# Optimization experiments

Measured on AMD Instinct MI355X. Metric: run time of the kernel, lower is better.

## Reference

```python
import jax, jax.numpy as jnp
import numpy as np

# ---- Cl(4,1) Cayley table (conformal GA: metric +,+,+,+,-) ----
_METRIC = (1.0, 1.0, 1.0, 1.0, -1.0)

def _reorder_sign(a, b):
    # sign from counting swaps to bring blade product to canonical order
    a >>= 1
    s = 0
    while a:
        s += bin(a & b).count("1")
        a >>= 1
    return -1.0 if (s & 1) else 1.0

def _build_cayley():
    C = np.zeros((32, 32, 32), dtype=np.float32)
    for a in range(32):
        for b in range(32):
            s = _reorder_sign(a, b)
            common = a & b
            for i in range(5):
                if (common >> i) & 1:
                    s *= _METRIC[i]
            C[a, b, a ^ b] += s
    return C

CAYLEY = _build_cayley()  # [32,32,32]; out_k = sum_ij C[i,j,k] x_i y_j

EPS = 1e-8

def normalize_cl41(x):
    n = jnp.sqrt(jnp.sum(x * x, axis=-1, keepdims=True))
    return x / (n + EPS)


def setup_inputs() -> dict:
    key = jax.random.key(0)
    k_x, k_wi, k_bi, k_wo, k_bo = jax.random.split(key, 5)
    B, S, D, H = 64, 2048, 6, 8
    x = jax.random.normal(k_x, (B, S, D), dtype=jnp.float32)
    W_in = jax.random.normal(k_wi, (D, H * 32), dtype=jnp.float32) * (1.0 / np.sqrt(D))
    b_in = jax.random.normal(k_bi, (H * 32,), dtype=jnp.float32) * 0.01
    W_out = jax.random.normal(k_wo, (H * 32, 32), dtype=jnp.float32) * (1.0 / np.sqrt(H * 32))
    b_out = jax.random.normal(k_bo, (32,), dtype=jnp.float32) * 0.01
    return {"x": x, "W_in": W_in, "b_in": b_in, "W_out": W_out, "b_out": b_out}


def reference(x, W_in, b_in, W_out, b_out):
    B, S, D = x.shape
    H = W_in.shape[1] // 32
    C = jnp.asarray(CAYLEY)
    # project inputs to per-channel multivectors: (B,S,H,32)
    u = (x @ W_in + b_in).reshape(B, S, H, 32)
    # initial rotor state: identity (scalar blade = 1)
    psi0 = jnp.zeros((B, H, 32), dtype=x.dtype).at[..., 0].set(1.0)

    def step(psi, u_t):  # u_t: (B,H,32)
        delta = normalize_cl41(u_t.at[..., 0].add(1.0))
        psi = normalize_cl41(jnp.einsum("bhi,bhj,ijk->bhk", delta, psi, C))
        return psi, psi

    _, psi_seq = jax.lax.scan(step, psi0, jnp.swapaxes(u, 0, 1))  # (S,B,H,32)
    out = normalize_cl41(psi_seq.reshape(S, B, H * 32) @ W_out + b_out)  # (S,B,32)
    return jnp.swapaxes(out, 0, 1)  # (B,S,32)
```

## Files before the change

### kernel.cpp

```cpp
#include <hip/hip_runtime.h>
#include <hip/hip_bf16.h>
#include <stdint.h>

#define BB 64
#define SS 2048
#define DD 6
#define HH 8
#define NCH 512
#define CHUNKS 256
#define LCH 8

typedef unsigned short ushort_t;
typedef __attribute__((ext_vector_type(8))) __bf16 bf16x8;
typedef __attribute__((ext_vector_type(4))) float f32x4;

struct SignTab { float s[32][32]; };

constexpr int popc5_c(unsigned v) {
    int c = 0;
    for (int i = 0; i < 5; ++i) c += (v >> i) & 1u;
    return c;
}

constexpr SignTab make_signs() {
    SignTab t{};
    for (int a = 0; a < 32; ++a) {
        for (int b = 0; b < 32; ++b) {
            int cnt = 0;
            unsigned aa = ((unsigned)a) >> 1;
            while (aa) { cnt += popc5_c(aa & (unsigned)b); aa >>= 1; }
            if ((a & b) & 16) cnt += 1;
            t.s[a][b] = (cnt & 1) ? -1.0f : 1.0f;
        }
    }
    return t;
}

constexpr SignTab SGN = make_signs();

__device__ __forceinline__ void gp_cl41(const float* __restrict__ a,
                                        const float* __restrict__ b,
                                        float* __restrict__ o) {
#pragma unroll
    for (int k = 0; k < 32; ++k) o[k] = 0.0f;
#pragma unroll
    for (int i = 0; i < 32; ++i) {
#pragma unroll
        for (int k = 0; k < 32; ++k) {
            o[k] = fmaf(SGN.s[i][i ^ k] * a[i], b[i ^ k], o[k]);
        }
    }
}

__device__ __forceinline__ float sumsq32(const float* v) {
    float n0 = 0.f, n1 = 0.f, n2 = 0.f, n3 = 0.f;
#pragma unroll
    for (int k = 0; k < 32; k += 4) {
        n0 = fmaf(v[k+0], v[k+0], n0);
        n1 = fmaf(v[k+1], v[k+1], n1);
        n2 = fmaf(v[k+2], v[k+2], n2);
        n3 = fmaf(v[k+3], v[k+3], n3);
    }
    return (n0 + n1) + (n2 + n3);
}

__device__ __forceinline__ float rsq(float n) {
    return __builtin_amdgcn_rsqf(n);
}

__device__ __forceinline__ uint32_t f2bf_rne(float f) {
    uint32_t u = __float_as_uint(f);
    return (u + 0x7FFFu + ((u >> 16) & 1u)) >> 16;
}

__device__ __forceinline__ uint32_t packh2(float a, float b) {
    union { _Float16 h[2]; uint32_t u; } t;
    t.h[0] = (_Float16)a; t.h[1] = (_Float16)b;
    return t.u;
}
__device__ __forceinline__ float h2lo(uint32_t u) {
    union { uint32_t u32; _Float16 h[2]; } t; t.u32 = u; return (float)t.h[0];
}
__device__ __forceinline__ float h2hi(uint32_t u) {
    union { uint32_t u32; _Float16 h[2]; } t; t.u32 = u; return (float)t.h[1];
}

__global__ __launch_bounds__(256) void k_local(
        const float* __restrict__ x, const float* __restrict__ W_in,
        const float* __restrict__ b_in, ushort_t* __restrict__ psi_loc,
        float* __restrict__ Tbuf) {
    __shared__ float4 sW4[8][57];
    for (int idx = threadIdx.x; idx < 8 * 56; idx += 256) {
        int h = idx / 56, r = idx % 56;
        float4 v;
        if (r < 48) {
            int d = r / 8, j4 = r % 8;
            const float* p = W_in + d * 256 + h * 32 + 4 * j4;
            v = make_float4(p[0], p[1], p[2], p[3]);
        } else {
            const float* p = b_in + h * 32 + 4 * (r - 48);
            v = make_float4(p[0], p[1], p[2], p[3]);
        }
        sW4[h][r] = v;
    }
    __syncthreads();

    int tid = blockIdx.x * 256 + threadIdx.x;
    int c  = tid >> 9;
    int bh = tid & 511;
    int b = bh >> 3, h = bh & 7;

    float4 bias4[8];
#pragma unroll
    for (int j4 = 0; j4 < 8; ++j4) bias4[j4] = sW4[h][48 + j4];

    float p[32];
#pragma unroll
    for (int k = 0; k < 32; ++k) p[k] = 0.f;
    p[0] = 1.f;

    const float* xrow = x + ((size_t)b * SS + (size_t)c * LCH) * DD;
    ushort_t* psi_base = psi_loc + (((size_t)b * SS + (size_t)c * LCH) * HH + h) * 32;

#pragma unroll 1
    for (int pr = 0; pr < LCH / 2; ++pr) {
        float xv[12];
#pragma unroll
        for (int d = 0; d < 6; ++d) {
            float2 t2 = *(const float2*)(xrow + 2 * d);
            xv[2 * d] = t2.x; xv[2 * d + 1] = t2.y;
        }
        xrow += 12;
        float x0[6], x1[6];
#pragma unroll
        for (int d = 0; d < 6; ++d) { x0[d] = xv[d]; x1[d] = xv[6 + d]; }

        float dl0[32], dl1[32];
#pragma unroll
        for (int j4 = 0; j4 < 8; ++j4) {
            float4 bv = bias4[j4];
            dl0[4*j4+0] = bv.x; dl0[4*j4+1] = bv.y; dl0[4*j4+2] = bv.z; dl0[4*j4+3] = bv.w;
            dl1[4*j4+0] = bv.x; dl1[4*j4+1] = bv.y; dl1[4*j4+2] = bv.z; dl1[4*j4+3] = bv.w;
        }
#pragma unroll
        for (int d = 0; d < 6; ++d) {
            float a0 = x0[d], a1 = x1[d];
#pragma unroll
            for (int j4 = 0; j4 < 8; ++j4) {
                float4 w = sW4[h][d * 8 + j4];
                dl0[4*j4+0] = fmaf(a0, w.x, dl0[4*j4+0]);
                dl0[4*j4+1] = fmaf(a0, w.y, dl0[4*j4+1]);
                dl0[4*j4+2] = fmaf(a0, w.z, dl0[4*j4+2]);
                dl0[4*j4+3] = fmaf(a0, w.w, dl0[4*j4+3]);
                dl1[4*j4+0] = fmaf(a1, w.x, dl1[4*j4+0]);
                dl1[4*j4+1] = fmaf(a1, w.y, dl1[4*j4+1]);
                dl1[4*j4+2] = fmaf(a1, w.z, dl1[4*j4+2]);
                dl1[4*j4+3] = fmaf(a1, w.w, dl1[4*j4+3]);
            }
        }
        dl0[0] += 1.0f;
        dl1[0] += 1.0f;

        float o[32];
        gp_cl41(dl0, p, o);
        {
            float inv = rsq(sumsq32(o));
            ushort_t* dst = psi_base + (size_t)(2 * pr) * HH * 32;
            uint32_t pk[16];
#pragma unroll
            for (int m = 0; m < 16; ++m)
                pk[m] = packh2(o[2*m] * inv, o[2*m+1] * inv);
            uint4* d4 = (uint4*)dst;
#pragma unroll
            for (int m = 0; m < 4; ++m)
                d4[m] = make_uint4(pk[4*m], pk[4*m+1], pk[4*m+2], pk[4*m+3]);
        }
        gp_cl41(dl1, o, p);
        {
            float inv = rsq(sumsq32(p));
            ushort_t* dst = psi_base + (size_t)(2 * pr + 1) * HH * 32;
            uint32_t pk[16];
#pragma unroll
            for (int m = 0; m < 16; ++m)
                pk[m] = packh2(p[2*m] * inv, p[2*m+1] * inv);
            uint4* d4 = (uint4*)dst;
#pragma unroll
            for (int m = 0; m < 4; ++m)
                d4[m] = make_uint4(pk[4*m], pk[4*m+1], pk[4*m+2], pk[4*m+3]);
        }
    }

    float inv = rsq(sumsq32(p));
    float* dst = Tbuf + ((size_t)bh * CHUNKS + c) * 32;
#pragma unroll
    for (int k = 0; k < 32; ++k) dst[k] = p[k] * inv;
}

__global__ __launch_bounds__(256) void k_scan_totals(
        const float* __restrict__ Tbuf, float* __restrict__ Ebuf) {
    __shared__ float sT[CHUNKS][33];
    int chain = blockIdx.x;
    int c = threadIdx.x;

    float v[32];
    const float* src = Tbuf + ((size_t)chain * CHUNKS + c) * 32;
#pragma unroll
    for (int k = 0; k < 32; ++k) { v[k] = src[k]; sT[c][k] = v[k]; }
    __syncthreads();

#pragma unroll 1
    for (int off = 1; off < CHUNKS; off <<= 1) {
        float w[32];
        bool act = (c >= off);
        if (act) {
#pragma unroll
            for (int k = 0; k < 32; ++k) w[k] = sT[c - off][k];
        }
        __syncthreads();
        if (act) {
            float o[32];
            gp_cl41(v, w, o);
            float inv = rsq(sumsq32(o));
#pragma unroll
            for (int k = 0; k < 32; ++k) { v[k] = o[k] * inv; sT[c][k] = v[k]; }
        }
        __syncthreads();
    }

    float* dst = Ebuf + (size_t)chain * CHUNKS * 32;
    if (c == 0) {
#pragma unroll
        for (int k = 0; k < 32; ++k) dst[k] = (k == 0) ? 1.f : 0.f;
    }
    if (c < CHUNKS - 1) {
        float* d2 = dst + (size_t)(c + 1) * 32;
#pragma unroll
        for (int k = 0; k < 32; ++k) d2[k] = v[k];
    }
}

__global__ __launch_bounds__(256) void k_fixup_proj(
        const ushort_t* __restrict__ psi_loc, const float* __restrict__ Ebuf,
        const float* __restrict__ W_out, const float* __restrict__ b_out,
        float* __restrict__ out) {
    int lane = threadIdx.x & 63;
    int wv = threadIdx.x >> 6;
    int q = lane >> 4;
    int n0 = lane & 15;

    bf16x8 Bf[2][8];
#pragma unroll
    for (int nt = 0; nt < 2; ++nt)
#pragma unroll
        for (int kk = 0; kk < 8; ++kk) {
            union { ushort_t u[8]; bf16x8 v; } tmp;
#pragma unroll
            for (int j = 0; j < 8; ++j)
                tmp.u[j] = (ushort_t)f2bf_rne(W_out[(kk * 32 + q * 8 + j) * 32 + nt * 16 + n0]);
            Bf[nt][kk] = tmp.v;
        }
    float bn0 = b_out[n0], bn1 = b_out[16 + n0];

    __shared__ ushort_t psiT[4][16][264];

#pragma unroll 1
    for (int tile = blockIdx.x * 4 + wv; tile < 8192; tile += 2048) {
        int rr0 = tile * 16;
        int b = rr0 >> 11;
        int s0 = rr0 & 2047;

        __syncthreads();

#pragma unroll
        for (int pp = 0; pp < 2; ++pp) {
            int row_local = pp * 8 + (lane >> 3);
            int h = lane & 7;
            int s = s0 + row_local;
            int c = s >> 3;
            int bh = b * 8 + h;

            float a[32], w[32], o[32];
            const uint4* pl = (const uint4*)(psi_loc +
                    (((size_t)b * SS + s) * HH + h) * 32);
#pragma unroll
            for (int m = 0; m < 4; ++m) {
                uint4 t4 = pl[m];
                uint32_t uu[4] = { t4.x, t4.y, t4.z, t4.w };
#pragma unroll
                for (int z = 0; z < 4; ++z) {
                    a[8*m + 2*z]     = h2lo(uu[z]);
                    a[8*m + 2*z + 1] = h2hi(uu[z]);
                }
            }
            const float* e = Ebuf + ((size_t)bh * CHUNKS + c) * 32;
#pragma unroll
            for (int k = 0; k < 32; ++k) w[k] = e[k];

            gp_cl41(a, w, o);
            float inv = rsq(sumsq32(o));

            uint32_t pk[16];
#pragma unroll
            for (int m = 0; m < 16; ++m)
                pk[m] = f2bf_rne(o[2*m] * inv) | (f2bf_rne(o[2*m+1] * inv) << 16);
            uint4* dst = (uint4*)&psiT[wv][row_local][h * 32];
#pragma unroll
            for (int m = 0; m < 4; ++m)
                dst[m] = make_uint4(pk[4*m], pk[4*m+1], pk[4*m+2], pk[4*m+3]);
        }

        __syncthreads();

        f32x4 acc0 = {0.f, 0.f, 0.f, 0.f};
        f32x4 acc1 = {0.f, 0.f, 0.f, 0.f};
#pragma unroll
        for (int kk = 0; kk < 8; ++kk) {
            bf16x8 af = *(const bf16x8*)&psiT[wv][n0][kk * 32 + q * 8];
            acc0 = __builtin_amdgcn_mfma_f32_16x16x32_bf16(af, Bf[0][kk], acc0, 0, 0, 0);
            acc1 = __builtin_amdgcn_mfma_f32_16x16x32_bf16(af, Bf[1][kk], acc1, 0, 0, 0);
        }

        float c0[4], c1[4], ss[4];
#pragma unroll
        for (int i = 0; i < 4; ++i) {
            c0[i] = acc0[i] + bn0;
            c1[i] = acc1[i] + bn1;
            ss[i] = c0[i] * c0[i] + c1[i] * c1[i];
        }
#pragma unroll
        for (int m = 1; m < 16; m <<= 1) {
#pragma unroll
            for (int i = 0; i < 4; ++i) ss[i] += __shfl_xor(ss[i], m);
        }
#pragma unroll
        for (int i = 0; i < 4; ++i) {
            float inv = rsq(ss[i]);
            int row = rr0 + q * 4 + i;
            out[(size_t)row * 32 + n0]      = c0[i] * inv;
            out[(size_t)row * 32 + 16 + n0] = c1[i] * inv;
        }
    }
}

extern "C" void kernel_launch(void* const* d_in, const int* in_sizes, int n_in,
                              void* d_out, int out_size, void* d_ws, size_t ws_size,
                              hipStream_t stream) {
    const float* x     = (const float*)d_in[0];
    const float* W_in  = (const float*)d_in[1];
    const float* b_in  = (const float*)d_in[2];
    const float* W_out = (const float*)d_in[3];
    const float* b_out = (const float*)d_in[4];
    float* out = (float*)d_out;

    char* ws = (char*)d_ws;
    float* Tbuf = (float*)ws;
    float* Ebuf = Tbuf;
    ushort_t* psi = (ushort_t*)(ws + (size_t)16 * 1024 * 1024);

    k_local      <<<512, 256, 0, stream>>>(x, W_in, b_in, psi, Tbuf);
    k_scan_totals<<<512, 256, 0, stream>>>(Tbuf, Ebuf);
    k_fixup_proj <<<512, 256, 0, stream>>>(psi, Ebuf, W_out, b_out, out);
}
```

Baseline: 204.0 us.

## Fuse local chunk scan into totals scan and recompute chains in projection kernel

The three-kernel pipeline becomes two. The first kernel computes each chunk's local product and the block-level prefix scan in one launch, so the Tbuf round trip is gone. The second kernel starts from the chunk prefix and recomputes the within-chunk chain, then feeds the results straight into the MFMA output projection. This removes the fp16 psi_loc intermediate, avoiding its global write and read and its precision loss, at the cost of running the geometric-product chain twice and adding more __syncthreads in small 64-thread blocks.

```diff
diff --git a/kernel.cpp b/kernel.cpp
--- a/kernel.cpp
+++ b/kernel.cpp
@@ -73,180 +73,179 @@
     return (u + 0x7FFFu + ((u >> 16) & 1u)) >> 16;
 }
 
-__device__ __forceinline__ uint32_t packh2(float a, float b) {
-    union { _Float16 h[2]; uint32_t u; } t;
-    t.h[0] = (_Float16)a; t.h[1] = (_Float16)b;
-    return t.u;
-}
-__device__ __forceinline__ float h2lo(uint32_t u) {
-    union { uint32_t u32; _Float16 h[2]; } t; t.u32 = u; return (float)t.h[0];
-}
-__device__ __forceinline__ float h2hi(uint32_t u) {
-    union { uint32_t u32; _Float16 h[2]; } t; t.u32 = u; return (float)t.h[1];
-}
-
-__global__ __launch_bounds__(256) void k_local(
+__device__ __forceinline__ void make_delta(const float4* __restrict__ sW,
+                                           const float* __restrict__ x6,
+                                           float* __restrict__ dl) {
+#pragma unroll
+    for (int j4 = 0; j4 < 8; ++j4) {
+        float4 bv = sW[48 + j4];
+        dl[4*j4+0] = bv.x; dl[4*j4+1] = bv.y; dl[4*j4+2] = bv.z; dl[4*j4+3] = bv.w;
+    }
+#pragma unroll
+    for (int d = 0; d < 6; ++d) {
+        float a = x6[d];
+#pragma unroll
+        for (int j4 = 0; j4 < 8; ++j4) {
+            float4 w = sW[d * 8 + j4];
+            dl[4*j4+0] = fmaf(a, w.x, dl[4*j4+0]);
+            dl[4*j4+1] = fmaf(a, w.y, dl[4*j4+1]);
+            dl[4*j4+2] = fmaf(a, w.z, dl[4*j4+2]);
+            dl[4*j4+3] = fmaf(a, w.w, dl[4*j4+3]);
+        }
+    }
+    dl[0] += 1.0f;
+}
+
+__global__ __launch_bounds__(256, 2) void k_scan(
         const float* __restrict__ x, const float* __restrict__ W_in,
-        const float* __restrict__ b_in, ushort_t* __restrict__ psi_loc,
-        float* __restrict__ Tbuf) {
+        const float* __restrict__ b_in, float* __restrict__ Ebuf) {
+    __shared__ float4 sW4[57];
+    __shared__ float sT[CHUNKS][36];
+
+    int chain = blockIdx.x;
+    int b = chain >> 3, h = chain & 7;
+    int c = threadIdx.x;
+
+    if (c < 56) {
+        float4 v;
+        if (c < 48) {
+            int d = c / 8, j4 = c % 8;
+            const float* p = W_in + d * 256 + h * 32 + 4 * j4;
+            v = make_float4(p[0], p[1], p[2], p[3]);
+        } else {
+            const float* p = b_in + h * 32 + 4 * (c - 48);
+            v = make_float4(p[0], p[1], p[2], p[3]);
+        }
+        sW4[c] = v;
+    }
+    __syncthreads();
+
+    const float* xrow = x + ((size_t)b * SS + (size_t)c * LCH) * DD;
+
+    float P[32], O[32], dl[32];
+
+    {
+        float xv[12];
+        const float4* xp = (const float4*)xrow;
+#pragma unroll
+        for (int m = 0; m < 3; ++m) {
+            float4 t4 = xp[m];
+            xv[4*m] = t4.x; xv[4*m+1] = t4.y; xv[4*m+2] = t4.z; xv[4*m+3] = t4.w;
+        }
+        make_delta(sW4, xv, O);
+        make_delta(sW4, xv + 6, dl);
+        gp_cl41(dl, O, P);
+    }
+#pragma unroll 1
+    for (int pr = 1; pr < 4; ++pr) {
+        float xv[12];
+        const float4* xp = (const float4*)(xrow + 12 * pr);
+#pragma unroll
+        for (int m = 0; m < 3; ++m) {
+            float4 t4 = xp[m];
+            xv[4*m] = t4.x; xv[4*m+1] = t4.y; xv[4*m+2] = t4.z; xv[4*m+3] = t4.w;
+        }
+        make_delta(sW4, xv, dl);
+        gp_cl41(dl, P, O);
+        make_delta(sW4, xv + 6, dl);
+        gp_cl41(dl, O, P);
+    }
+
+    float v[32];
+    {
+        float inv = rsq(sumsq32(P));
+#pragma unroll
+        for (int k = 0; k < 32; ++k) v[k] = P[k] * inv;
+#pragma unroll
+        for (int m = 0; m < 8; ++m)
+            *(float4*)&sT[c][4*m] = make_float4(v[4*m], v[4*m+1], v[4*m+2], v[4*m+3]);
+    }
+    __syncthreads();
+
+#pragma unroll 1
+    for (int off = 1; off < CHUNKS; off <<= 1) {
+        bool act = (c >= off);
+        if (act) {
+#pragma unroll
+            for (int m = 0; m < 8; ++m) {
+                float4 t4 = *(const float4*)&sT[c - off][4*m];
+                O[4*m] = t4.x; O[4*m+1] = t4.y; O[4*m+2] = t4.z; O[4*m+3] = t4.w;
+            }
+        }
+        __syncthreads();
+        if (act) {
+            gp_cl41(v, O, P);
+            float inv = rsq(sumsq32(P));
+#pragma unroll
+            for (int k = 0; k < 32; ++k) v[k] = P[k] * inv;
+#pragma unroll
+            for (int m = 0; m < 8; ++m)
+                *(float4*)&sT[c][4*m] = make_float4(v[4*m], v[4*m+1], v[4*m+2], v[4*m+3]);
+        }
+        __syncthreads();
+    }
+
+    float* dst = Ebuf + (size_t)chain * CHUNKS * 32;
+    if (c == 0) {
+        *(float4*)dst = make_float4(1.f, 0.f, 0.f, 0.f);
+#pragma unroll
+        for (int m = 1; m < 8; ++m) *(float4*)(dst + 4*m) = make_float4(0.f, 0.f, 0.f, 0.f);
+    }
+    if (c < CHUNKS - 1) {
+        float* d2 = dst + (size_t)(c + 1) * 32;
+#pragma unroll
+        for (int m = 0; m < 8; ++m)
+            *(float4*)(d2 + 4*m) = make_float4(v[4*m], v[4*m+1], v[4*m+2], v[4*m+3]);
+    }
+}
+
+__global__ __launch_bounds__(64, 2) void k_chain_proj(
+        const float* __restrict__ x, const float* __restrict__ W_in,
+        const float* __restrict__ b_in, const float* __restrict__ Ebuf,
+        const float* __restrict__ W_out, const float* __restrict__ b_out,
+        float* __restrict__ out) {
     __shared__ float4 sW4[8][57];
-    for (int idx = threadIdx.x; idx < 8 * 56; idx += 256) {
-        int h = idx / 56, r = idx % 56;
+    __shared__ float sX[384];
+    __shared__ ushort_t psiT[16][264];
+
+    int task = blockIdx.x;
+    int b = task >> 5, grp = task & 31;
+    int c0 = grp * 8;
+    int lane = threadIdx.x;
+    int cl = lane >> 3, h = lane & 7;
+    int q = lane >> 4, n0 = lane & 15;
+
+    for (int idx = lane; idx < 448; idx += 64) {
+        int hh = idx / 56, r = idx % 56;
         float4 v;
         if (r < 48) {
             int d = r / 8, j4 = r % 8;
-            const float* p = W_in + d * 256 + h * 32 + 4 * j4;
+            const float* p = W_in + d * 256 + hh * 32 + 4 * j4;
             v = make_float4(p[0], p[1], p[2], p[3]);
         } else {
-            const float* p = b_in + h * 32 + 4 * (r - 48);
+            const float* p = b_in + hh * 32 + 4 * (r - 48);
             v = make_float4(p[0], p[1], p[2], p[3]);
         }
-        sW4[h][r] = v;
-    }
-    __syncthreads();
-
-    int tid = blockIdx.x * 256 + threadIdx.x;
-    int c  = tid >> 9;
-    int bh = tid & 511;
-    int b = bh >> 3, h = bh & 7;
-
-    float4 bias4[8];
-#pragma unroll
-    for (int j4 = 0; j4 < 8; ++j4) bias4[j4] = sW4[h][48 + j4];
+        sW4[hh][r] = v;
+    }
+
+    {
+        const float2* xp = (const float2*)(x + ((size_t)b * SS + (size_t)c0 * LCH) * DD);
+        float2* sx2 = (float2*)sX;
+#pragma unroll
+        for (int m = 0; m < 3; ++m) sx2[lane * 3 + m] = xp[lane * 3 + m];
+    }
 
     float p[32];
-#pragma unroll
-    for (int k = 0; k < 32; ++k) p[k] = 0.f;
-    p[0] = 1.f;
-
-    const float* xrow = x + ((size_t)b * SS + (size_t)c * LCH) * DD;
-    ushort_t* psi_base = psi_loc + (((size_t)b * SS + (size_t)c * LCH) * HH + h) * 32;
-
-#pragma unroll 1
-    for (int pr = 0; pr < LCH / 2; ++pr) {
-        float xv[12];
-#pragma unroll
-        for (int d = 0; d < 6; ++d) {
-            float2 t2 = *(const float2*)(xrow + 2 * d);
-            xv[2 * d] = t2.x; xv[2 * d + 1] = t2.y;
-        }
-        xrow += 12;
-        float x0[6], x1[6];
-#pragma unroll
-        for (int d = 0; d < 6; ++d) { x0[d] = xv[d]; x1[d] = xv[6 + d]; }
-
-        float dl0[32], dl1[32];
-#pragma unroll
-        for (int j4 = 0; j4 < 8; ++j4) {
-            float4 bv = bias4[j4];
-            dl0[4*j4+0] = bv.x; dl0[4*j4+1] = bv.y; dl0[4*j4+2] = bv.z; dl0[4*j4+3] = bv.w;
-            dl1[4*j4+0] = bv.x; dl1[4*j4+1] = bv.y; dl1[4*j4+2] = bv.z; dl1[4*j4+3] = bv.w;
-        }
-#pragma unroll
-        for (int d = 0; d < 6; ++d) {
-            float a0 = x0[d], a1 = x1[d];
-#pragma unroll
-            for (int j4 = 0; j4 < 8; ++j4) {
-                float4 w = sW4[h][d * 8 + j4];
-                dl0[4*j4+0] = fmaf(a0, w.x, dl0[4*j4+0]);
-                dl0[4*j4+1] = fmaf(a0, w.y, dl0[4*j4+1]);
-                dl0[4*j4+2] = fmaf(a0, w.z, dl0[4*j4+2]);
-                dl0[4*j4+3] = fmaf(a0, w.w, dl0[4*j4+3]);
-                dl1[4*j4+0] = fmaf(a1, w.x, dl1[4*j4+0]);
-                dl1[4*j4+1] = fmaf(a1, w.y, dl1[4*j4+1]);
-                dl1[4*j4+2] = fmaf(a1, w.z, dl1[4*j4+2]);
-                dl1[4*j4+3] = fmaf(a1, w.w, dl1[4*j4+3]);
-            }
-        }
-        dl0[0] += 1.0f;
-        dl1[0] += 1.0f;
-
-        float o[32];
-        gp_cl41(dl0, p, o);
-        {
-            float inv = rsq(sumsq32(o));
-            ushort_t* dst = psi_base + (size_t)(2 * pr) * HH * 32;
-            uint32_t pk[16];
-#pragma unroll
-            for (int m = 0; m < 16; ++m)
-                pk[m] = packh2(o[2*m] * inv, o[2*m+1] * inv);
-            uint4* d4 = (uint4*)dst;
-#pragma unroll
-            for (int m = 0; m < 4; ++m)
-                d4[m] = make_uint4(pk[4*m], pk[4*m+1], pk[4*m+2], pk[4*m+3]);
-        }
-        gp_cl41(dl1, o, p);
-        {
-            float inv = rsq(sumsq32(p));
-            ushort_t* dst = psi_base + (size_t)(2 * pr + 1) * HH * 32;
-            uint32_t pk[16];
-#pragma unroll
-            for (int m = 0; m < 16; ++m)
-                pk[m] = packh2(p[2*m] * inv, p[2*m+1] * inv);
-            uint4* d4 = (uint4*)dst;
-#pragma unroll
-            for (int m = 0; m < 4; ++m)
-                d4[m] = make_uint4(pk[4*m], pk[4*m+1], pk[4*m+2], pk[4*m+3]);
-        }
-    }
-
-    float inv = rsq(sumsq32(p));
-    float* dst = Tbuf + ((size_t)bh * CHUNKS + c) * 32;
-#pragma unroll
-    for (int k = 0; k < 32; ++k) dst[k] = p[k] * inv;
-}
-
-__global__ __launch_bounds__(256) void k_scan_totals(
-        const float* __restrict__ Tbuf, float* __restrict__ Ebuf) {
-    __shared__ float sT[CHUNKS][33];
-    int chain = blockIdx.x;
-    int c = threadIdx.x;
-
-    float v[32];
-    const float* src = Tbuf + ((size_t)chain * CHUNKS + c) * 32;
-#pragma unroll
-    for (int k = 0; k < 32; ++k) { v[k] = src[k]; sT[c][k] = v[k]; }
-    __syncthreads();
-
-#pragma unroll 1
-    for (int off = 1; off < CHUNKS; off <<= 1) {
-        float w[32];
-        bool act = (c >= off);
-        if (act) {
-#pragma unroll
-            for (int k = 0; k < 32; ++k) w[k] = sT[c - off][k];
-        }
-        __syncthreads();
-        if (act) {
-            float o[32];
-            gp_cl41(v, w, o);
-            float inv = rsq(sumsq32(o));
-#pragma unroll
-            for (int k = 0; k < 32; ++k) { v[k] = o[k] * inv; sT[c][k] = v[k]; }
-        }
-        __syncthreads();
-    }
-
-    float* dst = Ebuf + (size_t)chain * CHUNKS * 32;
-    if (c == 0) {
-#pragma unroll
-        for (int k = 0; k < 32; ++k) dst[k] = (k == 0) ? 1.f : 0.f;
-    }
-    if (c < CHUNKS - 1) {
-        float* d2 = dst + (size_t)(c + 1) * 32;
-#pragma unroll
-        for (int k = 0; k < 32; ++k) d2[k] = v[k];
-    }
-}
-
-__global__ __launch_bounds__(256) void k_fixup_proj(
-        const ushort_t* __restrict__ psi_loc, const float* __restrict__ Ebuf,
-        const float* __restrict__ W_out, const float* __restrict__ b_out,
-        float* __restrict__ out) {
-    int lane = threadIdx.x & 63;
-    int wv = threadIdx.x >> 6;
-    int q = lane >> 4;
-    int n0 = lane & 15;
+    {
+        const float4* ep = (const float4*)(Ebuf +
+                (((size_t)b * HH + h) * CHUNKS + (c0 + cl)) * 32);
+#pragma unroll
+        for (int m = 0; m < 8; ++m) {
+            float4 t4 = ep[m];
+            p[4*m] = t4.x; p[4*m+1] = t4.y; p[4*m+2] = t4.z; p[4*m+3] = t4.w;
+        }
+    }
 
     bf16x8 Bf[2][8];
 #pragma unroll
@@ -261,53 +260,44 @@
         }
     float bn0 = b_out[n0], bn1 = b_out[16 + n0];
 
-    __shared__ ushort_t psiT[4][16][264];
+    __syncthreads();
 
 #pragma unroll 1
-    for (int tile = blockIdx.x * 4 + wv; tile < 8192; tile += 2048) {
-        int rr0 = tile * 16;
-        int b = rr0 >> 11;
-        int s0 = rr0 & 2047;
-
-        __syncthreads();
-
-#pragma unroll
-        for (int pp = 0; pp < 2; ++pp) {
-            int row_local = pp * 8 + (lane >> 3);
-            int h = lane & 7;
-            int s = s0 + row_local;
-            int c = s >> 3;
-            int bh = b * 8 + h;
-
-            float a[32], w[32], o[32];
-            const uint4* pl = (const uint4*)(psi_loc +
-                    (((size_t)b * SS + s) * HH + h) * 32);
-#pragma unroll
-            for (int m = 0; m < 4; ++m) {
-                uint4 t4 = pl[m];
-                uint32_t uu[4] = { t4.x, t4.y, t4.z, t4.w };
-#pragma unroll
-                for (int z = 0; z < 4; ++z) {
-                    a[8*m + 2*z]     = h2lo(uu[z]);
-                    a[8*m + 2*z + 1] = h2hi(uu[z]);
-                }
-            }
-            const float* e = Ebuf + ((size_t)bh * CHUNKS + c) * 32;
-#pragma unroll
-            for (int k = 0; k < 32; ++k) w[k] = e[k];
-
-            gp_cl41(a, w, o);
+    for (int pr = 0; pr < 4; ++pr) {
+        float x0[6], x1[6];
+#pragma unroll
+        for (int d = 0; d < 6; ++d) {
+            x0[d] = sX[(cl * 8 + 2 * pr) * 6 + d];
+            x1[d] = sX[(cl * 8 + 2 * pr + 1) * 6 + d];
+        }
+
+        float dl[32], o[32];
+        make_delta(sW4[h], x0, dl);
+        gp_cl41(dl, p, o);
+        {
             float inv = rsq(sumsq32(o));
-
             uint32_t pk[16];
 #pragma unroll
             for (int m = 0; m < 16; ++m)
                 pk[m] = f2bf_rne(o[2*m] * inv) | (f2bf_rne(o[2*m+1] * inv) << 16);
-            uint4* dst = (uint4*)&psiT[wv][row_local][h * 32];
+            uint4* dst = (uint4*)&psiT[cl * 2][h * 32];
 #pragma unroll
             for (int m = 0; m < 4; ++m)
                 dst[m] = make_uint4(pk[4*m], pk[4*m+1], pk[4*m+2], pk[4*m+3]);
         }
+        make_delta(sW4[h], x1, dl);
+        gp_cl41(dl, o, p);
+        {
+            float inv = rsq(sumsq32(p));
+            uint32_t pk[16];
+#pragma unroll
+            for (int m = 0; m < 16; ++m)
+                pk[m] = f2bf_rne(p[2*m] * inv) | (f2bf_rne(p[2*m+1] * inv) << 16);
+            uint4* dst = (uint4*)&psiT[cl * 2 + 1][h * 32];
+#pragma unroll
+            for (int m = 0; m < 4; ++m)
+                dst[m] = make_uint4(pk[4*m], pk[4*m+1], pk[4*m+2], pk[4*m+3]);
+        }
 
         __syncthreads();
 
@@ -315,30 +305,34 @@
         f32x4 acc1 = {0.f, 0.f, 0.f, 0.f};
 #pragma unroll
         for (int kk = 0; kk < 8; ++kk) {
-            bf16x8 af = *(const bf16x8*)&psiT[wv][n0][kk * 32 + q * 8];
+            bf16x8 af = *(const bf16x8*)&psiT[n0][kk * 32 + q * 8];
             acc0 = __builtin_amdgcn_mfma_f32_16x16x32_bf16(af, Bf[0][kk], acc0, 0, 0, 0);
             acc1 = __builtin_amdgcn_mfma_f32_16x16x32_bf16(af, Bf[1][kk], acc1, 0, 0, 0);
         }
 
-        float c0[4], c1[4], ss[4];
+        float c0v[4], c1v[4], ssq[4];
 #pragma unroll
         for (int i = 0; i < 4; ++i) {
-            c0[i] = acc0[i] + bn0;
-            c1[i] = acc1[i] + bn1;
-            ss[i] = c0[i] * c0[i] + c1[i] * c1[i];
+            c0v[i] = acc0[i] + bn0;
+            c1v[i] = acc1[i] + bn1;
+            ssq[i] = c0v[i] * c0v[i] + c1v[i] * c1v[i];
         }
 #pragma unroll
         for (int m = 1; m < 16; m <<= 1) {
 #pragma unroll
-            for (int i = 0; i < 4; ++i) ss[i] += __shfl_xor(ss[i], m);
+            for (int i = 0; i < 4; ++i) ssq[i] += __shfl_xor(ssq[i], m);
         }
 #pragma unroll
         for (int i = 0; i < 4; ++i) {
-            float inv = rsq(ss[i]);
-            int row = rr0 + q * 4 + i;
-            out[(size_t)row * 32 + n0]      = c0[i] * inv;
-            out[(size_t)row * 32 + 16 + n0] = c1[i] * inv;
-        }
+            float inv = rsq(ssq[i]);
+            int mrow = q * 4 + i;
+            int s = (c0 + (mrow >> 1)) * LCH + 2 * pr + (mrow & 1);
+            size_t row = (size_t)b * SS + s;
+            out[row * 32 + n0]      = c0v[i] * inv;
+            out[row * 32 + 16 + n0] = c1v[i] * inv;
+        }
+
+        __syncthreads();
     }
 }
 
@@ -352,12 +346,8 @@
     const float* b_out = (const float*)d_in[4];
     float* out = (float*)d_out;
 
-    char* ws = (char*)d_ws;
-    float* Tbuf = (float*)ws;
-    float* Ebuf = Tbuf;
-    ushort_t* psi = (ushort_t*)(ws + (size_t)16 * 1024 * 1024);
-
-    k_local      <<<512, 256, 0, stream>>>(x, W_in, b_in, psi, Tbuf);
-    k_scan_totals<<<512, 256, 0, stream>>>(Tbuf, Ebuf);
-    k_fixup_proj <<<512, 256, 0, stream>>>(psi, Ebuf, W_out, b_out, out);
-}
+    float* Ebuf = (float*)d_ws;
+
+    k_scan      <<<NCH,  256, 0, stream>>>(x, W_in, b_in, Ebuf);
+    k_chain_proj<<<2048,  64, 0, stream>>>(x, W_in, b_in, Ebuf, W_out, b_out, out);
+}
```

Result: slower. 240.5 us (+17.9%).
